# Performance work log

Hardware: AMD Instinct MI355X
Metric: run time of the kernel (lower is better)

The kernel has to match this reference:

```python
import jax, jax.numpy as jnp
import numpy as np

B, S, D, H = 2, 2048, 1024, 16
DEPTH = D // H
NEG = -1e9


def setup_inputs() -> dict:
    key = jax.random.key(0)
    ks = jax.random.split(key, 8)
    scale = 1.0 / np.sqrt(D)
    inp = {
        "query": jax.random.normal(ks[0], (B, S, D), jnp.float32),
        "key": jax.random.normal(ks[1], (B, S, D), jnp.float32),
        "value": jax.random.normal(ks[2], (B, S, D), jnp.float32),
        # causal look-ahead mask: 1 where attention is disallowed
        "mask": (1.0 - jnp.tril(jnp.ones((S, S), jnp.float32)))[None, None, :, :],
        "Wq": jax.random.normal(ks[3], (D, D), jnp.float32) * scale,
        "Wk": jax.random.normal(ks[4], (D, D), jnp.float32) * scale,
        "Wv": jax.random.normal(ks[5], (D, D), jnp.float32) * scale,
        "Wo": jax.random.normal(ks[6], (D, D), jnp.float32) * scale,
        "bq": jnp.zeros((D,), jnp.float32),
        "bk": jnp.zeros((D,), jnp.float32),
        "bv": jnp.zeros((D,), jnp.float32),
        "bo": jnp.zeros((D,), jnp.float32),
    }
    return inp


def _split_heads(x):
    # [B,S,D] -> [B,H,S,depth]
    return x.reshape(B, -1, H, DEPTH).transpose(0, 2, 1, 3)


def reference(query, key, value, mask, Wq, Wk, Wv, Wo, bq, bk, bv, bo):
    q = _split_heads(query @ Wq + bq)
    k = _split_heads(key @ Wk + bk)
    v = _split_heads(value @ Wv + bv)
    logits = jnp.einsum("bhqd,bhkd->bhqk", q, k) / jnp.sqrt(jnp.float32(DEPTH))
    logits = logits + mask * NEG
    attn = jax.nn.softmax(logits, axis=-1)
    ctx = jnp.einsum("bhqk,bhkd->bhqd", attn, v)  # [B,H,S,depth]
    concat = ctx.transpose(0, 2, 1, 3).reshape(B, -1, D)
    return concat @ Wo + bo
```

## Files before the change

### kernel.cpp

```cpp
#include <hip/hip_runtime.h>
#include <hip/hip_bf16.h>
#include <stdint.h>

#define BB 2
#define SS 2048
#define DDIM 1024
#define HH 16
#define DEPTH 64
#define MROWS (BB*SS)

typedef short bf16x8 __attribute__((ext_vector_type(8)));
typedef float f32x4 __attribute__((ext_vector_type(4)));

__device__ inline ushort f2bf(float f) {
  union { float f; unsigned u; } v; v.f = f;
  unsigned r = v.u + 0x7fffu + ((v.u >> 16) & 1u);
  return (ushort)(r >> 16);
}

__device__ inline uint pkbf(float a, float b) {
  uint r;
  asm("v_cvt_pk_bf16_f32 %0, %1, %2" : "=v"(r) : "v"(a), "v"(b));
  return r;
}

__device__ inline void gload_lds16(const void* g, void* l) {
  __builtin_amdgcn_global_load_lds(
      (const __attribute__((address_space(1))) unsigned*)g,
      (__attribute__((address_space(3))) unsigned*)l,
      16, 0, 0);
}

__global__ void wprep_kernel(const float* __restrict__ W0, const float* __restrict__ W1,
                             const float* __restrict__ W2, const float* __restrict__ W3,
                             ushort* __restrict__ T0, ushort* __restrict__ T1,
                             ushort* __restrict__ T2, ushort* __restrict__ T3) {
  __shared__ float tile[32][33];
  int z = blockIdx.x >> 10;
  int rr = blockIdx.x & 1023;
  const float* W = (z == 0) ? W0 : (z == 1) ? W1 : (z == 2) ? W2 : W3;
  ushort* T = (z == 0) ? T0 : (z == 1) ? T1 : (z == 2) ? T2 : T3;
  int tx = threadIdx.x & 31, ty = threadIdx.x >> 5;
  int n0 = (rr & 31) * 32, k0 = (rr >> 5) * 32;
#pragma unroll
  for (int i = 0; i < 4; i++)
    tile[ty + i * 8][tx] = W[(size_t)(k0 + ty + i * 8) * DDIM + n0 + tx];
  __syncthreads();
#pragma unroll
  for (int i = 0; i < 4; i++)
    T[(size_t)(n0 + ty + i * 8) * DDIM + k0 + tx] = f2bf(tile[tx][ty + i * 8]);
}

__global__ __launch_bounds__(256, 2) void qkv_gemm_kernel(
    const float* __restrict__ Aq, const float* __restrict__ Ak, const float* __restrict__ Av,
    const ushort* __restrict__ Wqt, const ushort* __restrict__ Wkt, const ushort* __restrict__ Wvt,
    const float* __restrict__ bqp, const float* __restrict__ bkp, const float* __restrict__ bvp,
    ushort* __restrict__ Qh, ushort* __restrict__ Kh, ushort* __restrict__ Vtg) {
  const int id = blockIdx.x;
  const int xcd = id & 7;
  const int rest = id >> 3;
  const int xblk = rest & 7;
  const int slot = rest >> 3;
  const int g = xcd * 12 + slot;
  const int yblk = g & 31;
  const int z = g >> 5;

  const float*  Ap = (z == 0) ? Aq  : (z == 1) ? Ak  : Av;
  const ushort* Bt = (z == 0) ? Wqt : (z == 1) ? Wkt : Wvt;
  const float* bias = (z == 0) ? bqp : (z == 1) ? bkp : bvp;

  __shared__ __align__(16) ushort As[2][128 * 64];
  __shared__ __align__(16) ushort Bs[2][128 * 64];
  const int tid = threadIdx.x;
  const int w = tid >> 6, lane = tid & 63;
  const int m0 = yblk * 128, n0 = xblk * 128;
  const int wr = (w >> 1) * 64, wc = (w & 1) * 64;
  const int l4 = lane >> 4, l15 = lane & 15;
  const int row16 = tid >> 4;
  const int col4 = (tid & 15) * 4;
  const int acolw = col4 ^ ((row16 & 7) << 3);
  const int srow8 = w * 8 + (lane >> 3);
  const int bcolg = (((lane & 7) ^ (lane >> 3)) << 3);
  const int fswz = (l15 & 7) << 3;

  f32x4 zero = {0.f, 0.f, 0.f, 0.f};
  f32x4 acc[4][4];
#pragma unroll
  for (int i = 0; i < 4; i++)
#pragma unroll
    for (int j = 0; j < 4; j++) acc[i][j] = zero;

  float4 areg[8];
#pragma unroll
  for (int j = 0; j < 8; ++j)
    areg[j] = *(const float4*)&Ap[(size_t)(m0 + j * 16 + row16) * DDIM + col4];
#pragma unroll
  for (int it = 0; it < 4; ++it)
    gload_lds16(Bt + (size_t)(n0 + it * 32 + srow8) * DDIM + bcolg,
                &Bs[0][(it * 32 + w * 8) * 64]);
#pragma unroll
  for (int j = 0; j < 8; ++j) {
    uint2 pk;
    pk.x = pkbf(areg[j].x, areg[j].y);
    pk.y = pkbf(areg[j].z, areg[j].w);
    *(uint2*)&As[0][(j * 16 + row16) * 64 + acolw] = pk;
  }
#pragma unroll
  for (int j = 0; j < 8; ++j)
    areg[j] = *(const float4*)&Ap[(size_t)(m0 + j * 16 + row16) * DDIM + 64 + col4];
  __syncthreads();

  int buf = 0;
  for (int t = 0; t < 16; ++t) {
    if (t + 1 < 16) {
#pragma unroll
      for (int it = 0; it < 4; ++it)
        gload_lds16(Bt + (size_t)(n0 + it * 32 + srow8) * DDIM + (t + 1) * 64 + bcolg,
                    &Bs[buf ^ 1][(it * 32 + w * 8) * 64]);
#pragma unroll
      for (int j = 0; j < 8; ++j) {
        uint2 pk;
        pk.x = pkbf(areg[j].x, areg[j].y);
        pk.y = pkbf(areg[j].z, areg[j].w);
        *(uint2*)&As[buf ^ 1][(j * 16 + row16) * 64 + acolw] = pk;
      }
      if (t + 2 < 16) {
#pragma unroll
        for (int j = 0; j < 8; ++j)
          areg[j] = *(const float4*)&Ap[(size_t)(m0 + j * 16 + row16) * DDIM + (t + 2) * 64 + col4];
      }
    }
#pragma unroll
    for (int kk = 0; kk < 2; ++kk) {
      bf16x8 af[4], bfr[4];
#pragma unroll
      for (int m = 0; m < 4; m++)
        af[m] = *(const bf16x8*)&As[buf][(wr + m * 16 + l15) * 64 + ((kk * 32 + l4 * 8) ^ fswz)];
#pragma unroll
      for (int n = 0; n < 4; n++)
        bfr[n] = *(const bf16x8*)&Bs[buf][(wc + n * 16 + l15) * 64 + ((kk * 32 + l4 * 8) ^ fswz)];
#pragma unroll
      for (int m = 0; m < 4; m++)
#pragma unroll
        for (int n = 0; n < 4; n++)
          acc[m][n] = __builtin_amdgcn_mfma_f32_16x16x32_bf16(af[m], bfr[n], acc[m][n], 0, 0, 0);
    }
    __syncthreads();
    buf ^= 1;
  }

  if (z != 2) {
    ushort* outp = (z == 0) ? Qh : Kh;
    ushort* wtile = (w < 2) ? &As[0][w * 4096] : &As[1][(w - 2) * 4096];
    const int gcol0 = n0 + wc;
    const int hh = gcol0 >> 6;
    const int bb = m0 >> 11;
    const int s0g = (m0 + wr) & (SS - 1);
#pragma unroll
    for (int m = 0; m < 4; m++) {
#pragma unroll
      for (int n = 0; n < 4; n++) {
        int dloc = n * 16 + l15;
        float bv = bias[gcol0 + dloc];
#pragma unroll
        for (int r = 0; r < 4; r++) {
          int sloc = m * 16 + l4 * 4 + r;
          wtile[sloc * 64 + (dloc ^ ((sloc & 7) << 3))] = f2bf(acc[m][n][r] + bv);
        }
      }
    }
#pragma unroll
    for (int i = 0; i < 8; ++i) {
      int srow = i * 8 + (lane >> 3);
      int dch = (lane & 7) * 8;
      bf16x8 val = *(const bf16x8*)&wtile[srow * 64 + (dch ^ ((srow & 7) << 3))];
      *(bf16x8*)&outp[((size_t)(bb * HH + hh) * SS + s0g + srow) * DEPTH + dch] = val;
    }
  } else {
    ushort* wtile = (w < 2) ? &As[0][w * 2048] : &As[1][(w - 2) * 2048];
    const int gcol0 = n0 + wc;
    const int hh = gcol0 >> 6;
    const int bb = m0 >> 11;
    const int s0g = (m0 + wr) & (SS - 1);
#pragma unroll
    for (int p = 0; p < 2; ++p) {
#pragma unroll
      for (int nn = 0; nn < 2; ++nn) {
        int n = p * 2 + nn;
        int dloc = nn * 16 + l15;
        float bv = bias[gcol0 + p * 32 + dloc];
#pragma unroll
        for (int m = 0; m < 4; m++) {
#pragma unroll
          for (int rr = 0; rr < 4; rr += 2) {
            int sloc = m * 16 + l4 * 4 + rr;
            int gg = (sloc >> 3) ^ (dloc & 7);
            uint pk = pkbf(acc[m][n][rr] + bv, acc[m][n][rr + 1] + bv);
            *(uint*)&wtile[dloc * 64 + gg * 8 + (sloc & 7)] = pk;
          }
        }
      }
      __syncthreads();
#pragma unroll
      for (int i = 0; i < 4; ++i) {
        int dloc = (lane >> 3) + i * 8;
        int gg = (lane & 7) ^ (dloc & 7);
        bf16x8 val = *(const bf16x8*)&wtile[dloc * 64 + gg * 8];
        int dglob = p * 32 + dloc;
        size_t addr = ((size_t)(bb * HH + hh) * DEPTH + dglob) * SS + s0g + (lane & 7) * 8;
        *(bf16x8*)&Vtg[addr] = val;
      }
      __syncthreads();
    }
  }
}

__global__ __launch_bounds__(256, 3) void out_gemm_kernel(
    const ushort* __restrict__ A, const ushort* __restrict__ Bt,
    const float* __restrict__ bias, float* __restrict__ out,
    int M, int N, int K) {
  __shared__ __align__(16) ushort As[2][128 * 64];
  __shared__ __align__(16) ushort Bs[2][64 * 64];
  const int id = blockIdx.x;
  const int xcd = id & 7;
  const int rest = id >> 3;
  const int xblk = rest & 15;
  const int slot = rest >> 4;
  const int yblk = xcd * 4 + slot;

  const int tid = threadIdx.x;
  const int w = tid >> 6, lane = tid & 63;
  const int m0 = yblk * 128, n0 = xblk * 64;
  const int wr = (w >> 1) * 64, wc = (w & 1) * 32;
  const int l4 = lane >> 4, l15 = lane & 15;
  const int srow8 = w * 8 + (lane >> 3);
  const int scolg = (((lane & 7) ^ (lane >> 3)) << 3);
  const int fswz = (l15 & 7) << 3;

  f32x4 zero = {0.f, 0.f, 0.f, 0.f};
  f32x4 acc[4][2];
#pragma unroll
  for (int i = 0; i < 4; i++)
#pragma unroll
    for (int j = 0; j < 2; j++) acc[i][j] = zero;

#pragma unroll
  for (int it = 0; it < 4; ++it)
    gload_lds16(A + (size_t)(m0 + it * 32 + srow8) * K + scolg,
                &As[0][(it * 32 + w * 8) * 64]);
#pragma unroll
  for (int it = 0; it < 2; ++it)
    gload_lds16(Bt + (size_t)(n0 + it * 32 + srow8) * K + scolg,
                &Bs[0][(it * 32 + w * 8) * 64]);
  __syncthreads();

  int buf = 0;
  for (int t = 0; t < 16; ++t) {
    if (t + 1 < 16) {
#pragma unroll
      for (int it = 0; it < 4; ++it)
        gload_lds16(A + (size_t)(m0 + it * 32 + srow8) * K + (t + 1) * 64 + scolg,
                    &As[buf ^ 1][(it * 32 + w * 8) * 64]);
#pragma unroll
      for (int it = 0; it < 2; ++it)
        gload_lds16(Bt + (size_t)(n0 + it * 32 + srow8) * K + (t + 1) * 64 + scolg,
                    &Bs[buf ^ 1][(it * 32 + w * 8) * 64]);
    }
#pragma unroll
    for (int kk = 0; kk < 2; ++kk) {
      bf16x8 af[4], bfr[2];
#pragma unroll
      for (int m = 0; m < 4; m++)
        af[m] = *(const bf16x8*)&As[buf][(wr + m * 16 + l15) * 64 + ((kk * 32 + l4 * 8) ^ fswz)];
#pragma unroll
      for (int n = 0; n < 2; n++)
        bfr[n] = *(const bf16x8*)&Bs[buf][(wc + n * 16 + l15) * 64 + ((kk * 32 + l4 * 8) ^ fswz)];
#pragma unroll
      for (int m = 0; m < 4; m++)
#pragma unroll
        for (int n = 0; n < 2; n++)
          acc[m][n] = __builtin_amdgcn_mfma_f32_16x16x32_bf16(af[m], bfr[n], acc[m][n], 0, 0, 0);
    }
    __syncthreads();
    buf ^= 1;
  }

#pragma unroll
  for (int m = 0; m < 4; m++) {
#pragma unroll
    for (int n = 0; n < 2; n++) {
      int col = n0 + wc + n * 16 + l15;
      float bv = bias[col];
#pragma unroll
      for (int r = 0; r < 4; r++) {
        int row = m0 + wr + m * 16 + l4 * 4 + r;
        out[(size_t)row * N + col] = acc[m][n][r] + bv;
      }
    }
  }
}

__global__ __launch_bounds__(256, 4) void attn_kernel(
    const ushort* __restrict__ Qh, const ushort* __restrict__ Kh,
    const ushort* __restrict__ Vt, ushort* __restrict__ ctx) {
  __shared__ __align__(16) ushort Ks[2][64 * 64];
  __shared__ __align__(16) ushort Vs[2][64 * 64];
  __shared__ __align__(16) ushort Ps[4][16 * 64];
  const int tid = threadIdx.x;
  const int w = tid >> 6, lane = tid & 63;
  const int l4 = lane >> 4, l15 = lane & 15;
  const float CE = 0.18033688f;

  const int xcd = blockIdx.x & 7;
  const int local = blockIdx.x >> 3;
  const int bh = xcd * 4 + (local & 3);
  const int chunk = 31 - (local >> 2);
  const int b = bh >> 4, h = bh & 15;
  const size_t qkbase = (size_t)bh * SS * DEPTH;
  const size_t vbase  = (size_t)bh * DEPTH * SS;

  const int srow_w = w * 8 + (lane >> 3);
  const int colb_lin = (lane & 7) * 16;
  const int swz_rd = (l15 & 7) << 3;

  const int q0 = chunk * 64 + w * 16;
  const int nt = chunk + 1;

  const int krow0 = srow_w;
  const int kcol  = (colb_lin ^ ((krow0 & 7) << 4)) >> 1;
  const ushort* kp0 = Kh + qkbase + (size_t)krow0 * DEPTH + kcol;
  const ushort* kp1 = kp0 + 32 * DEPTH;
  const ushort* vp0 = Vt + vbase + (size_t)krow0 * SS + kcol;
  const ushort* vp1 = vp0 + 32 * SS;
  const int lds0 = w * 512;
  const int lds1 = 2048 + w * 512;

  bf16x8 aq[2];
#pragma unroll
  for (int cc = 0; cc < 2; cc++)
    aq[cc] = *(const bf16x8*)&Qh[qkbase + (size_t)(q0 + l15) * DEPTH + cc * 32 + l4 * 8];

  f32x4 zero = {0.f, 0.f, 0.f, 0.f};
  f32x4 o[4];
  float m_run = -__builtin_inff(), l_run = 0.f;
#pragma unroll
  for (int d = 0; d < 4; d++) o[d] = zero;

  int buf = 0;
  gload_lds16(kp0, &Ks[0][lds0]);
  gload_lds16(vp0, &Vs[0][lds0]);
  gload_lds16(kp1, &Ks[0][lds1]);
  gload_lds16(vp1, &Vs[0][lds1]);
  kp0 += 64 * DEPTH; kp1 += 64 * DEPTH; vp0 += 64; vp1 += 64;
  __syncthreads();

  for (int t = 0; t < nt; ++t) {
    if (t + 1 < nt) {
      gload_lds16(kp0, &Ks[buf ^ 1][lds0]);
      gload_lds16(vp0, &Vs[buf ^ 1][lds0]);
      gload_lds16(kp1, &Ks[buf ^ 1][lds1]);
      gload_lds16(vp1, &Vs[buf ^ 1][lds1]);
      kp0 += 64 * DEPTH; kp1 += 64 * DEPTH; vp0 += 64; vp1 += 64;
    }

    const int kv0 = t * 64;
    f32x4 s[4];
    __builtin_amdgcn_s_setprio(1);
#pragma unroll
    for (int n = 0; n < 4; n++) {
      f32x4 zacc = zero;
      int kr = n * 16 + l15;
#pragma unroll
      for (int cc = 0; cc < 2; cc++) {
        bf16x8 bk = *(const bf16x8*)&Ks[buf][kr * 64 + ((cc * 32 + l4 * 8) ^ swz_rd)];
        zacc = __builtin_amdgcn_mfma_f32_16x16x32_bf16(bk, aq[cc], zacc, 0, 0, 0);
      }
      s[n] = zacc;
    }
    __builtin_amdgcn_s_setprio(0);

    const int qg = q0 + l15;
    if (t == nt - 1) {
#pragma unroll
      for (int n = 0; n < 4; n++) {
        int kb = kv0 + n * 16 + l4 * 4;
#pragma unroll
        for (int r = 0; r < 4; r++)
          if (kb + r > qg) s[n][r] = -1e9f;
      }
    }

    float mx = fmaxf(fmaxf(s[0][0], s[0][1]), s[0][2]);
    mx = fmaxf(fmaxf(mx, s[0][3]), s[1][0]);
    mx = fmaxf(fmaxf(mx, s[1][1]), s[1][2]);
    mx = fmaxf(fmaxf(mx, s[1][3]), s[2][0]);
    mx = fmaxf(fmaxf(mx, s[2][1]), s[2][2]);
    mx = fmaxf(fmaxf(mx, s[2][3]), s[3][0]);
    mx = fmaxf(fmaxf(mx, s[3][1]), s[3][2]);
    mx = fmaxf(mx, s[3][3]);
    mx = fmaxf(mx, __shfl_xor(mx, 16));
    mx = fmaxf(mx, __shfl_xor(mx, 32));
    if (!__all(mx - m_run <= 44.36f)) {
      float mnew = fmaxf(m_run, mx);
      float alpha = exp2f((m_run - mnew) * CE);
      m_run = mnew;
      l_run *= alpha;
#pragma unroll
      for (int d = 0; d < 4; d++) o[d] *= alpha;
    }
    float mc = m_run * CE;
    float rs = 0.f;
#pragma unroll
    for (int n = 0; n < 4; n++)
#pragma unroll
      for (int r = 0; r < 4; r++) {
        float p = exp2f(s[n][r] * CE - mc);
        s[n][r] = p;
        rs += p;
      }
    l_run += rs;

    ushort* Pw = &Ps[w][0];
#pragma unroll
    for (int n = 0; n < 4; n++) {
      int col = (n * 16 + l4 * 4) ^ swz_rd;
      uint2 pk;
      pk.x = pkbf(s[n][0], s[n][1]);
      pk.y = pkbf(s[n][2], s[n][3]);
      *(uint2*)&Pw[l15 * 64 + col] = pk;
    }

    bf16x8 pa[2];
#pragma unroll
    for (int cc = 0; cc < 2; cc++)
      pa[cc] = *(const bf16x8*)&Pw[l15 * 64 + ((cc * 32 + l4 * 8) ^ swz_rd)];

    __builtin_amdgcn_s_setprio(1);
#pragma unroll
    for (int d = 0; d < 4; d++) {
      int dr = d * 16 + l15;
#pragma unroll
      for (int cc = 0; cc < 2; cc++) {
        bf16x8 av = *(const bf16x8*)&Vs[buf][dr * 64 + ((cc * 32 + l4 * 8) ^ swz_rd)];
        o[d] = __builtin_amdgcn_mfma_f32_16x16x32_bf16(av, pa[cc], o[d], 0, 0, 0);
      }
    }
    __builtin_amdgcn_s_setprio(0);

    __syncthreads();
    buf ^= 1;
  }

  float lv = l_run;
  lv += __shfl_xor(lv, 16);
  lv += __shfl_xor(lv, 32);
  float inv = 1.f / lv;
  size_t rowbase = ((size_t)(b * SS + q0 + l15)) * DDIM + h * DEPTH;
#pragma unroll
  for (int d = 0; d < 4; d++) {
    *(uint*)&ctx[rowbase + d * 16 + l4 * 4]     = pkbf(o[d][0] * inv, o[d][1] * inv);
    *(uint*)&ctx[rowbase + d * 16 + l4 * 4 + 2] = pkbf(o[d][2] * inv, o[d][3] * inv);
  }
}

extern "C" void kernel_launch(void* const* d_in, const int* in_sizes, int n_in,
                              void* d_out, int out_size, void* d_ws, size_t ws_size,
                              hipStream_t stream) {
  const float* query = (const float*)d_in[0];
  const float* key_  = (const float*)d_in[1];
  const float* value = (const float*)d_in[2];
  const float* Wq = (const float*)d_in[4];
  const float* Wk = (const float*)d_in[5];
  const float* Wv = (const float*)d_in[6];
  const float* Wo = (const float*)d_in[7];
  const float* bq = (const float*)d_in[8];
  const float* bk = (const float*)d_in[9];
  const float* bv = (const float*)d_in[10];
  const float* bo = (const float*)d_in[11];

  char* ws = (char*)d_ws;
  const size_t MB = 1u << 20;
  ushort* Wqt = (ushort*)(ws + 24 * MB);
  ushort* Wkt = (ushort*)(ws + 26 * MB);
  ushort* Wvt = (ushort*)(ws + 28 * MB);
  ushort* Wot = (ushort*)(ws + 30 * MB);
  ushort* Qh  = (ushort*)(ws + 32 * MB);
  ushort* Kh  = (ushort*)(ws + 40 * MB);
  ushort* Vtg = (ushort*)(ws + 48 * MB);
  ushort* Cb  = (ushort*)(ws + 56 * MB);

  wprep_kernel<<<4096, 256, 0, stream>>>(Wq, Wk, Wv, Wo, Wqt, Wkt, Wvt, Wot);

  qkv_gemm_kernel<<<768, 256, 0, stream>>>(
      query, key_, value, Wqt, Wkt, Wvt, bq, bk, bv, Qh, Kh, Vtg);

  attn_kernel<<<1024, 256, 0, stream>>>(Qh, Kh, Vtg, Cb);

  out_gemm_kernel<<<512, 256, 0, stream>>>(
      Cb, Wot, bo, (float*)d_out, MROWS, DDIM, DDIM);
}
```

Baseline: 115.7 us.

## Pre-convert QKV activations to bf16 and use async LDS loads with smaller tiles

Adds a conversion pass to the prep kernel that casts the query, key and value activations to bf16 in the workspace. The QKV GEMM can then load A directly with global_load_lds instead of register-staged fp32 loads plus packing. The GEMM tile shrinks from 128x128 to 128x64 with more blocks and occupancy 3, and the LDS-staged epilogue becomes direct scattered global stores. The cost is an extra full read and write of the activations, plus less coalesced output stores.

Result: no change. 116.1 us (+0.4%).

```diff
diff --git a/kernel.cpp b/kernel.cpp
--- a/kernel.cpp
+++ b/kernel.cpp
@@ -31,83 +31,87 @@
       16, 0, 0);
 }
 
-__global__ void wprep_kernel(const float* __restrict__ W0, const float* __restrict__ W1,
-                             const float* __restrict__ W2, const float* __restrict__ W3,
-                             ushort* __restrict__ T0, ushort* __restrict__ T1,
-                             ushort* __restrict__ T2, ushort* __restrict__ T3) {
+__global__ void prep_kernel(const float* __restrict__ q, const float* __restrict__ k,
+                            const float* __restrict__ v,
+                            ushort* __restrict__ xq, ushort* __restrict__ xk,
+                            ushort* __restrict__ xv,
+                            const float* __restrict__ W0, const float* __restrict__ W1,
+                            const float* __restrict__ W2, const float* __restrict__ W3,
+                            ushort* __restrict__ T0, ushort* __restrict__ T1,
+                            ushort* __restrict__ T2, ushort* __restrict__ T3) {
   __shared__ float tile[32][33];
-  int z = blockIdx.x >> 10;
-  int rr = blockIdx.x & 1023;
-  const float* W = (z == 0) ? W0 : (z == 1) ? W1 : (z == 2) ? W2 : W3;
-  ushort* T = (z == 0) ? T0 : (z == 1) ? T1 : (z == 2) ? T2 : T3;
-  int tx = threadIdx.x & 31, ty = threadIdx.x >> 5;
-  int n0 = (rr & 31) * 32, k0 = (rr >> 5) * 32;
-#pragma unroll
-  for (int i = 0; i < 4; i++)
-    tile[ty + i * 8][tx] = W[(size_t)(k0 + ty + i * 8) * DDIM + n0 + tx];
-  __syncthreads();
-#pragma unroll
-  for (int i = 0; i < 4; i++)
-    T[(size_t)(n0 + ty + i * 8) * DDIM + k0 + tx] = f2bf(tile[tx][ty + i * 8]);
-}
-
-__global__ __launch_bounds__(256, 2) void qkv_gemm_kernel(
-    const float* __restrict__ Aq, const float* __restrict__ Ak, const float* __restrict__ Av,
+  if (blockIdx.x < 6144) {
+    int z = blockIdx.x >> 11;
+    const float* in = (z == 0) ? q : (z == 1) ? k : v;
+    ushort* out = (z == 0) ? xq : (z == 1) ? xk : xv;
+    int i = (blockIdx.x & 2047) * 256 + threadIdx.x;
+    const float4* p = (const float4*)in + (size_t)i * 2;
+    float4 a = p[0], b = p[1];
+    uint tmp[4] = { pkbf(a.x, a.y), pkbf(a.z, a.w), pkbf(b.x, b.y), pkbf(b.z, b.w) };
+    *(uint4*)(out + (size_t)i * 8) = *(uint4*)tmp;
+  } else {
+    int idx = blockIdx.x - 6144;
+    int z = idx >> 10;
+    int rr = idx & 1023;
+    const float* W = (z == 0) ? W0 : (z == 1) ? W1 : (z == 2) ? W2 : W3;
+    ushort* T = (z == 0) ? T0 : (z == 1) ? T1 : (z == 2) ? T2 : T3;
+    int tx = threadIdx.x & 31, ty = threadIdx.x >> 5;
+    int n0 = (rr & 31) * 32, k0 = (rr >> 5) * 32;
+#pragma unroll
+    for (int i = 0; i < 4; i++)
+      tile[ty + i * 8][tx] = W[(size_t)(k0 + ty + i * 8) * DDIM + n0 + tx];
+    __syncthreads();
+#pragma unroll
+    for (int i = 0; i < 4; i++)
+      T[(size_t)(n0 + ty + i * 8) * DDIM + k0 + tx] = f2bf(tile[tx][ty + i * 8]);
+  }
+}
+
+__global__ __launch_bounds__(256, 3) void qkv_gemm_kernel(
+    const ushort* __restrict__ Xq, const ushort* __restrict__ Xk, const ushort* __restrict__ Xv,
     const ushort* __restrict__ Wqt, const ushort* __restrict__ Wkt, const ushort* __restrict__ Wvt,
     const float* __restrict__ bqp, const float* __restrict__ bkp, const float* __restrict__ bvp,
     ushort* __restrict__ Qh, ushort* __restrict__ Kh, ushort* __restrict__ Vtg) {
+  __shared__ __align__(16) ushort As[2][128 * 64];
+  __shared__ __align__(16) ushort Bs[2][64 * 64];
   const int id = blockIdx.x;
   const int xcd = id & 7;
   const int rest = id >> 3;
-  const int xblk = rest & 7;
-  const int slot = rest >> 3;
-  const int g = xcd * 12 + slot;
+  const int xblk = rest & 15;
+  const int gslot = rest >> 4;
+  const int g = xcd * 12 + gslot;
   const int yblk = g & 31;
   const int z = g >> 5;
 
-  const float*  Ap = (z == 0) ? Aq  : (z == 1) ? Ak  : Av;
+  const ushort* A  = (z == 0) ? Xq  : (z == 1) ? Xk  : Xv;
   const ushort* Bt = (z == 0) ? Wqt : (z == 1) ? Wkt : Wvt;
   const float* bias = (z == 0) ? bqp : (z == 1) ? bkp : bvp;
-
-  __shared__ __align__(16) ushort As[2][128 * 64];
-  __shared__ __align__(16) ushort Bs[2][128 * 64];
+  const int K = DDIM;
+
   const int tid = threadIdx.x;
   const int w = tid >> 6, lane = tid & 63;
-  const int m0 = yblk * 128, n0 = xblk * 128;
-  const int wr = (w >> 1) * 64, wc = (w & 1) * 64;
+  const int m0 = yblk * 128, n0 = xblk * 64;
+  const int wr = (w >> 1) * 64, wc = (w & 1) * 32;
   const int l4 = lane >> 4, l15 = lane & 15;
-  const int row16 = tid >> 4;
-  const int col4 = (tid & 15) * 4;
-  const int acolw = col4 ^ ((row16 & 7) << 3);
   const int srow8 = w * 8 + (lane >> 3);
-  const int bcolg = (((lane & 7) ^ (lane >> 3)) << 3);
+  const int scolg = (((lane & 7) ^ (lane >> 3)) << 3);
   const int fswz = (l15 & 7) << 3;
 
   f32x4 zero = {0.f, 0.f, 0.f, 0.f};
-  f32x4 acc[4][4];
+  f32x4 acc[4][2];
 #pragma unroll
   for (int i = 0; i < 4; i++)
 #pragma unroll
-    for (int j = 0; j < 4; j++) acc[i][j] = zero;
-
-  float4 areg[8];
-#pragma unroll
-  for (int j = 0; j < 8; ++j)
-    areg[j] = *(const float4*)&Ap[(size_t)(m0 + j * 16 + row16) * DDIM + col4];
+    for (int j = 0; j < 2; j++) acc[i][j] = zero;
+
 #pragma unroll
   for (int it = 0; it < 4; ++it)
-    gload_lds16(Bt + (size_t)(n0 + it * 32 + srow8) * DDIM + bcolg,
+    gload_lds16(A + (size_t)(m0 + it * 32 + srow8) * K + scolg,
+                &As[0][(it * 32 + w * 8) * 64]);
+#pragma unroll
+  for (int it = 0; it < 2; ++it)
+    gload_lds16(Bt + (size_t)(n0 + it * 32 + srow8) * K + scolg,
                 &Bs[0][(it * 32 + w * 8) * 64]);
-#pragma unroll
-  for (int j = 0; j < 8; ++j) {
-    uint2 pk;
-    pk.x = pkbf(areg[j].x, areg[j].y);
-    pk.y = pkbf(areg[j].z, areg[j].w);
-    *(uint2*)&As[0][(j * 16 + row16) * 64 + acolw] = pk;
-  }
-#pragma unroll
-  for (int j = 0; j < 8; ++j)
-    areg[j] = *(const float4*)&Ap[(size_t)(m0 + j * 16 + row16) * DDIM + 64 + col4];
   __syncthreads();
 
   int buf = 0;
@@ -115,102 +119,61 @@
     if (t + 1 < 16) {
 #pragma unroll
       for (int it = 0; it < 4; ++it)
-        gload_lds16(Bt + (size_t)(n0 + it * 32 + srow8) * DDIM + (t + 1) * 64 + bcolg,
+        gload_lds16(A + (size_t)(m0 + it * 32 + srow8) * K + (t + 1) * 64 + scolg,
+                    &As[buf ^ 1][(it * 32 + w * 8) * 64]);
+#pragma unroll
+      for (int it = 0; it < 2; ++it)
+        gload_lds16(Bt + (size_t)(n0 + it * 32 + srow8) * K + (t + 1) * 64 + scolg,
                     &Bs[buf ^ 1][(it * 32 + w * 8) * 64]);
-#pragma unroll
-      for (int j = 0; j < 8; ++j) {
-        uint2 pk;
-        pk.x = pkbf(areg[j].x, areg[j].y);
-        pk.y = pkbf(areg[j].z, areg[j].w);
-        *(uint2*)&As[buf ^ 1][(j * 16 + row16) * 64 + acolw] = pk;
-      }
-      if (t + 2 < 16) {
-#pragma unroll
-        for (int j = 0; j < 8; ++j)
-          areg[j] = *(const float4*)&Ap[(size_t)(m0 + j * 16 + row16) * DDIM + (t + 2) * 64 + col4];
-      }
     }
 #pragma unroll
     for (int kk = 0; kk < 2; ++kk) {
-      bf16x8 af[4], bfr[4];
+      bf16x8 af[4], bfr[2];
 #pragma unroll
       for (int m = 0; m < 4; m++)
         af[m] = *(const bf16x8*)&As[buf][(wr + m * 16 + l15) * 64 + ((kk * 32 + l4 * 8) ^ fswz)];
 #pragma unroll
-      for (int n = 0; n < 4; n++)
+      for (int n = 0; n < 2; n++)
         bfr[n] = *(const bf16x8*)&Bs[buf][(wc + n * 16 + l15) * 64 + ((kk * 32 + l4 * 8) ^ fswz)];
 #pragma unroll
       for (int m = 0; m < 4; m++)
 #pragma unroll
-        for (int n = 0; n < 4; n++)
+        for (int n = 0; n < 2; n++)
           acc[m][n] = __builtin_amdgcn_mfma_f32_16x16x32_bf16(af[m], bfr[n], acc[m][n], 0, 0, 0);
     }
     __syncthreads();
     buf ^= 1;
   }
 
+  const int hh = n0 >> 6;
+  const int bb = m0 >> 11;
+  const int s0g = (m0 + wr) & (SS - 1);
   if (z != 2) {
     ushort* outp = (z == 0) ? Qh : Kh;
-    ushort* wtile = (w < 2) ? &As[0][w * 4096] : &As[1][(w - 2) * 4096];
-    const int gcol0 = n0 + wc;
-    const int hh = gcol0 >> 6;
-    const int bb = m0 >> 11;
-    const int s0g = (m0 + wr) & (SS - 1);
 #pragma unroll
     for (int m = 0; m < 4; m++) {
 #pragma unroll
-      for (int n = 0; n < 4; n++) {
-        int dloc = n * 16 + l15;
-        float bv = bias[gcol0 + dloc];
+      for (int n = 0; n < 2; n++) {
+        int dloc = wc + n * 16 + l15;
+        float bv = bias[n0 + dloc];
 #pragma unroll
         for (int r = 0; r < 4; r++) {
-          int sloc = m * 16 + l4 * 4 + r;
-          wtile[sloc * 64 + (dloc ^ ((sloc & 7) << 3))] = f2bf(acc[m][n][r] + bv);
+          int s = s0g + m * 16 + l4 * 4 + r;
+          outp[((size_t)(bb * HH + hh) * SS + s) * DEPTH + dloc] = f2bf(acc[m][n][r] + bv);
         }
       }
     }
-#pragma unroll
-    for (int i = 0; i < 8; ++i) {
-      int srow = i * 8 + (lane >> 3);
-      int dch = (lane & 7) * 8;
-      bf16x8 val = *(const bf16x8*)&wtile[srow * 64 + (dch ^ ((srow & 7) << 3))];
-      *(bf16x8*)&outp[((size_t)(bb * HH + hh) * SS + s0g + srow) * DEPTH + dch] = val;
-    }
   } else {
-    ushort* wtile = (w < 2) ? &As[0][w * 2048] : &As[1][(w - 2) * 2048];
-    const int gcol0 = n0 + wc;
-    const int hh = gcol0 >> 6;
-    const int bb = m0 >> 11;
-    const int s0g = (m0 + wr) & (SS - 1);
-#pragma unroll
-    for (int p = 0; p < 2; ++p) {
-#pragma unroll
-      for (int nn = 0; nn < 2; ++nn) {
-        int n = p * 2 + nn;
-        int dloc = nn * 16 + l15;
-        float bv = bias[gcol0 + p * 32 + dloc];
-#pragma unroll
-        for (int m = 0; m < 4; m++) {
-#pragma unroll
-          for (int rr = 0; rr < 4; rr += 2) {
-            int sloc = m * 16 + l4 * 4 + rr;
-            int gg = (sloc >> 3) ^ (dloc & 7);
-            uint pk = pkbf(acc[m][n][rr] + bv, acc[m][n][rr + 1] + bv);
-            *(uint*)&wtile[dloc * 64 + gg * 8 + (sloc & 7)] = pk;
-          }
-        }
-      }
-      __syncthreads();
-#pragma unroll
-      for (int i = 0; i < 4; ++i) {
-        int dloc = (lane >> 3) + i * 8;
-        int gg = (lane & 7) ^ (dloc & 7);
-        bf16x8 val = *(const bf16x8*)&wtile[dloc * 64 + gg * 8];
-        int dglob = p * 32 + dloc;
-        size_t addr = ((size_t)(bb * HH + hh) * DEPTH + dglob) * SS + s0g + (lane & 7) * 8;
-        *(bf16x8*)&Vtg[addr] = val;
-      }
-      __syncthreads();
+#pragma unroll
+    for (int m = 0; m < 4; m++) {
+#pragma unroll
+      for (int n = 0; n < 2; n++) {
+        int dloc = wc + n * 16 + l15;
+        float bv = bias[n0 + dloc];
+        size_t rowb = ((size_t)(bb * HH + hh) * DEPTH + dloc) * SS + s0g + m * 16 + l4 * 4;
+        *(uint*)&Vtg[rowb]     = pkbf(acc[m][n][0] + bv, acc[m][n][1] + bv);
+        *(uint*)&Vtg[rowb + 2] = pkbf(acc[m][n][2] + bv, acc[m][n][3] + bv);
+      }
     }
   }
 }
@@ -480,6 +443,9 @@
 
   char* ws = (char*)d_ws;
   const size_t MB = 1u << 20;
+  ushort* Xq  = (ushort*)(ws + 0 * MB);
+  ushort* Xk  = (ushort*)(ws + 8 * MB);
+  ushort* Xv  = (ushort*)(ws + 16 * MB);
   ushort* Wqt = (ushort*)(ws + 24 * MB);
   ushort* Wkt = (ushort*)(ws + 26 * MB);
   ushort* Wvt = (ushort*)(ws + 28 * MB);
@@ -489,10 +455,11 @@
   ushort* Vtg = (ushort*)(ws + 48 * MB);
   ushort* Cb  = (ushort*)(ws + 56 * MB);
 
-  wprep_kernel<<<4096, 256, 0, stream>>>(Wq, Wk, Wv, Wo, Wqt, Wkt, Wvt, Wot);
-
-  qkv_gemm_kernel<<<768, 256, 0, stream>>>(
-      query, key_, value, Wqt, Wkt, Wvt, bq, bk, bv, Qh, Kh, Vtg);
+  prep_kernel<<<6144 + 4096, 256, 0, stream>>>(query, key_, value, Xq, Xk, Xv,
+                                               Wq, Wk, Wv, Wo, Wqt, Wkt, Wvt, Wot);
+
+  qkv_gemm_kernel<<<1536, 256, 0, stream>>>(
+      Xq, Xk, Xv, Wqt, Wkt, Wvt, bq, bk, bv, Qh, Kh, Vtg);
 
   attn_kernel<<<1024, 256, 0, stream>>>(Qh, Kh, Vtg, Cb);
 
```
